# Performance work log

Hardware: AMD Instinct MI355X
Metric: run time of the kernel (lower is better)

## Reference

```python
import jax, jax.numpy as jnp
import numpy as np

KE2 = 2.31e-4  # ke2 constant from source
EPS = 1e-12    # safe-norm epsilon
N = 4096


def setup_inputs() -> dict:
    key = jax.random.key(0)
    ks = jax.random.split(key, 16)
    f32 = jnp.float32
    inp = {}
    inp['positions'] = jax.random.normal(ks[0], (N, 3), f32) * 5.0
    inp['charges'] = jax.random.normal(ks[1], (N,), f32)
    inp['bond_coeffs'] = jax.random.uniform(ks[2], (7, 7), f32)
    inp['bond_lengths'] = jax.random.uniform(ks[3], (7, 7), f32)
    inp['angle_coeffs'] = jax.random.uniform(ks[4], (7, 7, 7), f32)
    inp['thetas'] = jax.random.uniform(ks[5], (7, 7, 7), f32)
    inp['dihedral_coeffs'] = jax.random.uniform(ks[6], (7, 7), f32)
    inp['phis'] = jax.random.uniform(ks[7], (7, 7), f32)
    inp['multiplicity'] = jax.random.uniform(ks[8], (7, 7), f32)
    inp['lj_E'] = jax.random.uniform(ks[9], (4, 4), f32)
    inp['lj_r'] = jax.random.uniform(ks[10], (4, 4), f32)
    inp['atom_types'] = jax.random.randint(ks[11], (N,), 0, 7)
    inp['lj_types'] = jax.random.randint(ks[12], (N,), 0, 4)
    inp['bond_idx'] = jax.random.randint(ks[13], (N, 2), 0, N)
    inp['angle_idx'] = jax.random.randint(ks[14], (2 * N, 3), 0, N)
    inp['dihedral_idx'] = jax.random.randint(ks[15], (3 * N, 4), 0, N)
    return inp


def _norm(v):
    return jnp.sqrt(jnp.sum(v * v, axis=-1) + EPS)


def reference(positions, charges, bond_coeffs, bond_lengths, angle_coeffs,
              thetas, dihedral_coeffs, phis, multiplicity, lj_E, lj_r,
              atom_types, lj_types, bond_idx, angle_idx, dihedral_idx):
    t = atom_types
    # ---- bond energy: 0.5*k*(|ri-rj| - r0)^2, vectorized gather + reduce
    b1, b2 = bond_idx[:, 0], bond_idx[:, 1]
    d = _norm(positions[b1] - positions[b2])
    e_bond = jnp.sum(0.5 * bond_coeffs[t[b1], t[b2]] * (d - bond_lengths[t[b1], t[b2]]) ** 2)
    # ---- angle energy: 0.5*k*(acos(cos) - theta0)^2
    a1, a2, a3 = angle_idx[:, 0], angle_idx[:, 1], angle_idx[:, 2]
    v1 = positions[a1] - positions[a2]
    v2 = positions[a3] - positions[a2]
    cos_a = jnp.sum(v1 * v2, -1) / (_norm(v1) * _norm(v2))
    ang = jnp.arccos(jnp.clip(cos_a, -1.0 + 1e-7, 1.0 - 1e-7))
    ta1, ta2, ta3 = t[a1], t[a2], t[a3]
    e_angle = jnp.sum(0.5 * angle_coeffs[ta1, ta2, ta3] * (ang - thetas[ta1, ta2, ta3]) ** 2)
    # ---- dihedral energy: 0.5*k*(1 + cos(n*phi - delta))
    d1, d2i, d3, d4 = (dihedral_idx[:, k] for k in range(4))
    w1 = positions[d2i] - positions[d1]
    w2 = positions[d3] - positions[d2i]
    w3 = positions[d4] - positions[d3]
    n1 = jnp.cross(w1, w2)
    n2 = jnp.cross(w2, w3)
    cos_d = jnp.sum(n1 * n2, -1) / (_norm(n1) * _norm(n2))
    sin_d = jnp.sum(jnp.cross(n1, n2) * w2, -1) / (_norm(w2) * _norm(n1) * _norm(n2))
    phi = jnp.arctan2(sin_d, cos_d)
    td2, td3 = t[d2i], t[d3]
    e_dih = jnp.sum(0.5 * dihedral_coeffs[td2, td3] *
                    (1.0 + jnp.cos(multiplicity[td2, td3] * phi - phis[td2, td3])))
    # ---- pairwise distance map (cdist) via gram trick, upper-triangle i<j mask
    n = positions.shape[0]
    sq = jnp.sum(positions * positions, -1)
    d2m = jnp.maximum(sq[:, None] + sq[None, :] - 2.0 * (positions @ positions.T), 0.0)
    idx = jnp.arange(n)
    mask = idx[:, None] < idx[None, :]
    r = jnp.sqrt(jnp.where(mask, d2m, 1.0) + EPS)  # [N,N], safe off-mask
    # ---- Lennard-Jones: 4*eps*((sig/r)^12 - (sig/r)^6)
    eps_ij = lj_E[lj_types[:, None], lj_types[None, :]]
    sig_ij = lj_r[lj_types[:, None], lj_types[None, :]]
    r6 = (sig_ij / r) ** 6
    e_lj = jnp.sum(jnp.where(mask, 4.0 * eps_ij * (r6 * r6 - r6), 0.0))
    # ---- Coulomb: ke2 * qi*qj / r
    e_c = jnp.sum(jnp.where(mask, KE2 * charges[:, None] * charges[None, :] / r, 0.0))
    return e_bond + e_angle + e_dih + e_lj + e_c
```

## Files before the change

### kernel.cpp

```cpp
#include <hip/hip_runtime.h>

#define NATOMS 4096
#define TILE   128
#define NTILES (NATOMS / TILE)
#define KE2F   0.000231f

#define NEAR_D2 1.0f

__global__ __launch_bounds__(256) void energy_kernel(
    const float* __restrict__ pos,
    const float* __restrict__ charges,
    const float* __restrict__ bond_coeffs,
    const float* __restrict__ bond_lengths,
    const float* __restrict__ angle_coeffs,
    const float* __restrict__ thetas,
    const float* __restrict__ dihedral_coeffs,
    const float* __restrict__ phis,
    const float* __restrict__ multiplicity,
    const float* __restrict__ lj_E,
    const float* __restrict__ lj_r,
    const int* __restrict__ atom_types,
    const int* __restrict__ lj_types,
    const int* __restrict__ bond_idx,
    const int* __restrict__ angle_idx,
    const int* __restrict__ dihedral_idx,
    float* __restrict__ out)
{
    const int bi  = blockIdx.y;
    const int bj  = blockIdx.x;
    const int tid = threadIdx.x;

    __shared__ float4 sp[TILE];
    __shared__ float  ssq[TILE];
    __shared__ int    st[TILE];
    __shared__ double red[4];

    double acc = 0.0;

    if (bj >= bi) {
        const int il   = tid & (TILE - 1);
        const int half = tid >> 7;
        const int ig   = bi * TILE + il;
        const int jb   = bj * TILE;

        if (tid < TILE) {
            const int jg = jb + tid;
            const float x = pos[jg*3+0], y = pos[jg*3+1], z = pos[jg*3+2];
            sp[tid]  = make_float4(x, y, z, charges[jg]);
            ssq[tid] = __fadd_rn(__fadd_rn(__fmul_rn(x,x), __fmul_rn(y,y)), __fmul_rn(z,z));
            st[tid]  = lj_types[jg];
        }

        const float xi = pos[ig*3+0], yi = pos[ig*3+1], zi = pos[ig*3+2];
        const float sqi = __fadd_rn(__fadd_rn(__fmul_rn(xi,xi), __fmul_rn(yi,yi)), __fmul_rn(zi,zi));
        const float aqi = __fmul_rn(KE2F, charges[ig]);
        const int   ti  = lj_types[ig];
        const float e0 = 4.f*lj_E[ti*4+0], e1 = 4.f*lj_E[ti*4+1],
                    e2 = 4.f*lj_E[ti*4+2], e3 = 4.f*lj_E[ti*4+3];
        const float s0 = lj_r[ti*4+0], s1 = lj_r[ti*4+1],
                    s2 = lj_r[ti*4+2], s3 = lj_r[ti*4+3];

        __syncthreads();

        const int j0 = half * (TILE/2);
        for (int jj = j0; jj < j0 + TILE/2; ++jj) {
            const float4 pj  = sp[jj];
            const float  sqj = ssq[jj];
            const int    tj  = st[jj];
            const int    jg  = jb + jj;
            const bool valid = jg > ig;

            const float dot = __fmaf_rn(zi, pj.z,
                              __fmaf_rn(yi, pj.y,
                              __fmaf_rn(xi, pj.x, 0.0f)));
            const float t   = __fadd_rn(sqi, sqj);
            const float d2  = __fsub_rn(t, __fmul_rn(2.0f, dot));
            const float d2m = fmaxf(d2, 0.0f);
            const float rr2 = __fadd_rn(d2m, 1e-12f);

            const float sig = (tj==0)?s0:(tj==1)?s1:(tj==2)?s2:s3;
            const float e4  = (tj==0)?e0:(tj==1)?e1:(tj==2)?e2:e3;

            if (__builtin_expect(d2m <= NEAR_D2, 0)) {
                if (valid) {
                    const float rf = __fsqrt_rn(rr2);
                    const float qv = __fdiv_rn(sig, rf);
                    const double u  = (double)qv;
                    const double u3 = u*u*u;
                    const float r6 = (float)(u3*u3);
                    const float lj = __fsub_rn(__fmul_rn(r6, r6), r6);
                    const float ljt = __fmul_rn(e4, lj);
                    const float cl  = __fdiv_rn(__fmul_rn(aqi, pj.w), rf);
                    acc += (double)ljt;
                    acc += (double)cl;
                }
            } else {
                const float invr = __builtin_amdgcn_rsqf(rr2);
                const float u  = sig * invr;
                const float u2 = u*u;
                const float u6 = u2*u2*u2;
                const float term = e4 * (u6*u6 - u6) + aqi * pj.w * invr;
                acc += valid ? (double)term : 0.0;
            }
        }
    } else {
        const int l   = (bi * (bi - 1)) / 2 + bj;
        const int NB  = NATOMS;
        const int NA  = 2 * NATOMS;
        const int ND  = 3 * NATOMS;
        const int TOT = NB + NA + ND;
        if (l * 256 >= TOT) return;
        const int item = l * 256 + tid;

        if (item < NB) {
            const int b1 = bond_idx[item*2+0];
            const int b2 = bond_idx[item*2+1];
            const float dx = pos[b1*3+0] - pos[b2*3+0];
            const float dy = pos[b1*3+1] - pos[b2*3+1];
            const float dz = pos[b1*3+2] - pos[b2*3+2];
            const float d  = sqrtf(dx*dx + dy*dy + dz*dz + 1e-12f);
            const int k    = atom_types[b1]*7 + atom_types[b2];
            const float dd = d - bond_lengths[k];
            acc = 0.5 * (double)(bond_coeffs[k] * dd * dd);
        } else if (item < NB + NA) {
            const int ai = item - NB;
            const int a1 = angle_idx[ai*3+0];
            const int a2 = angle_idx[ai*3+1];
            const int a3 = angle_idx[ai*3+2];
            const float v1x = pos[a1*3+0] - pos[a2*3+0];
            const float v1y = pos[a1*3+1] - pos[a2*3+1];
            const float v1z = pos[a1*3+2] - pos[a2*3+2];
            const float v2x = pos[a3*3+0] - pos[a2*3+0];
            const float v2y = pos[a3*3+1] - pos[a2*3+1];
            const float v2z = pos[a3*3+2] - pos[a2*3+2];
            const float n1 = sqrtf(v1x*v1x + v1y*v1y + v1z*v1z + 1e-12f);
            const float n2 = sqrtf(v2x*v2x + v2y*v2y + v2z*v2z + 1e-12f);
            float cosa = (v1x*v2x + v1y*v2y + v1z*v2z) / (n1 * n2);
            cosa = fminf(fmaxf(cosa, -1.0f + 1e-7f), 1.0f - 1e-7f);
            const float ang = acosf(cosa);
            const int k = atom_types[a1]*49 + atom_types[a2]*7 + atom_types[a3];
            const float dt = ang - thetas[k];
            acc = 0.5 * (double)(angle_coeffs[k] * dt * dt);
        } else {
            const int di = item - NB - NA;
            const int q1 = dihedral_idx[di*4+0];
            const int q2 = dihedral_idx[di*4+1];
            const int q3 = dihedral_idx[di*4+2];
            const int q4 = dihedral_idx[di*4+3];
            const float w1x = pos[q2*3+0] - pos[q1*3+0];
            const float w1y = pos[q2*3+1] - pos[q1*3+1];
            const float w1z = pos[q2*3+2] - pos[q1*3+2];
            const float w2x = pos[q3*3+0] - pos[q2*3+0];
            const float w2y = pos[q3*3+1] - pos[q2*3+1];
            const float w2z = pos[q3*3+2] - pos[q2*3+2];
            const float w3x = pos[q4*3+0] - pos[q3*3+0];
            const float w3y = pos[q4*3+1] - pos[q3*3+1];
            const float w3z = pos[q4*3+2] - pos[q3*3+2];
            const float n1x = w1y*w2z - w1z*w2y;
            const float n1y = w1z*w2x - w1x*w2z;
            const float n1z = w1x*w2y - w1y*w2x;
            const float n2x = w2y*w3z - w2z*w3y;
            const float n2y = w2z*w3x - w2x*w3z;
            const float n2z = w2x*w3y - w2y*w3x;
            const float nn1 = sqrtf(n1x*n1x + n1y*n1y + n1z*n1z + 1e-12f);
            const float nn2 = sqrtf(n2x*n2x + n2y*n2y + n2z*n2z + 1e-12f);
            const float nw2 = sqrtf(w2x*w2x + w2y*w2y + w2z*w2z + 1e-12f);
            const float cosd = (n1x*n2x + n1y*n2y + n1z*n2z) / (nn1 * nn2);
            const float cx = n1y*n2z - n1z*n2y;
            const float cy = n1z*n2x - n1x*n2z;
            const float cz = n1x*n2y - n1y*n2x;
            const float sind = (cx*w2x + cy*w2y + cz*w2z) / (nw2 * nn1 * nn2);
            const float phi = atan2f(sind, cosd);
            const int k = atom_types[q2]*7 + atom_types[q3];
            const float e = 0.5f * dihedral_coeffs[k]
                          * (1.0f + cosf(multiplicity[k]*phi - phis[k]));
            acc = (double)e;
        }
    }

    #pragma unroll
    for (int s = 32; s > 0; s >>= 1) acc += __shfl_down(acc, s, 64);
    if ((tid & 63) == 0) red[tid >> 6] = acc;
    __syncthreads();
    if (tid == 0) {
        const float tot = (float)(red[0] + red[1] + red[2] + red[3]);
        atomicAdd(out, tot);
    }
}

extern "C" void kernel_launch(void* const* d_in, const int* in_sizes, int n_in,
                              void* d_out, int out_size, void* d_ws, size_t ws_size,
                              hipStream_t stream) {
    (void)in_sizes; (void)n_in; (void)d_ws; (void)ws_size; (void)out_size;
    hipMemsetAsync(d_out, 0, sizeof(float), stream);
    dim3 grid(NTILES, NTILES);
    energy_kernel<<<grid, 256, 0, stream>>>(
        (const float*)d_in[0],  (const float*)d_in[1],
        (const float*)d_in[2],  (const float*)d_in[3],
        (const float*)d_in[4],  (const float*)d_in[5],
        (const float*)d_in[6],  (const float*)d_in[7],
        (const float*)d_in[8],  (const float*)d_in[9],
        (const float*)d_in[10], (const int*)d_in[11],
        (const int*)d_in[12],   (const int*)d_in[13],
        (const int*)d_in[14],   (const int*)d_in[15],
        (float*)d_out);
}
```

Before: 104.6 us.

## Use direct-difference distances, float accumulation, and tighter near-field threshold in pair loop

The pair loop now computes squared distance from coordinate differences rather than the gram expansion, and evaluates the exact gram-based path only when d2 falls below a much smaller threshold. Far-field contributions are summed into a float accumulator instead of double, and the validity test becomes a local index comparison. The inner loop is unrolled by 8 and the shared per-atom squared-norm array is removed. This cuts double-precision adds and branch divergence in the hot loop, at the cost of float-accumulation rounding error and possible mismatch with the reference's gram-trick distances near the threshold.

```diff
diff --git a/kernel.cpp b/kernel.cpp
--- a/kernel.cpp
+++ b/kernel.cpp
@@ -5,7 +5,7 @@
 #define NTILES (NATOMS / TILE)
 #define KE2F   0.000231f
 
-#define NEAR_D2 1.0f
+#define NEAR_D2 4e-3f
 
 __global__ __launch_bounds__(256) void energy_kernel(
     const float* __restrict__ pos,
@@ -31,78 +31,82 @@
     const int tid = threadIdx.x;
 
     __shared__ float4 sp[TILE];
-    __shared__ float  ssq[TILE];
     __shared__ int    st[TILE];
     __shared__ double red[4];
 
     double acc = 0.0;
 
     if (bj >= bi) {
-        const int il   = tid & (TILE - 1);
-        const int half = tid >> 7;
-        const int ig   = bi * TILE + il;
-        const int jb   = bj * TILE;
+        const int il  = tid & (TILE - 1);
+        const int sub = tid >> 7;
+        const int ig  = bi * TILE + il;
+        const int jb  = bj * TILE;
 
         if (tid < TILE) {
             const int jg = jb + tid;
-            const float x = pos[jg*3+0], y = pos[jg*3+1], z = pos[jg*3+2];
-            sp[tid]  = make_float4(x, y, z, charges[jg]);
-            ssq[tid] = __fadd_rn(__fadd_rn(__fmul_rn(x,x), __fmul_rn(y,y)), __fmul_rn(z,z));
-            st[tid]  = lj_types[jg];
+            sp[tid] = make_float4(pos[jg*3+0], pos[jg*3+1], pos[jg*3+2], charges[jg]);
+            st[tid] = lj_types[jg];
         }
 
         const float xi = pos[ig*3+0], yi = pos[ig*3+1], zi = pos[ig*3+2];
-        const float sqi = __fadd_rn(__fadd_rn(__fmul_rn(xi,xi), __fmul_rn(yi,yi)), __fmul_rn(zi,zi));
+        const float sqi = __fadd_rn(__fadd_rn(__fmul_rn(xi,xi), __fmul_rn(yi,yi)),
+                                    __fmul_rn(zi,zi));
         const float aqi = __fmul_rn(KE2F, charges[ig]);
         const int   ti  = lj_types[ig];
         const float e0 = 4.f*lj_E[ti*4+0], e1 = 4.f*lj_E[ti*4+1],
                     e2 = 4.f*lj_E[ti*4+2], e3 = 4.f*lj_E[ti*4+3];
         const float s0 = lj_r[ti*4+0], s1 = lj_r[ti*4+1],
                     s2 = lj_r[ti*4+2], s3 = lj_r[ti*4+3];
+        const int jmin = (bi == bj) ? il : -1;
 
         __syncthreads();
 
-        const int j0 = half * (TILE/2);
+        float accf = 0.0f;
+        const int j0 = sub * (TILE/2);
+        #pragma unroll 8
         for (int jj = j0; jj < j0 + TILE/2; ++jj) {
-            const float4 pj  = sp[jj];
-            const float  sqj = ssq[jj];
-            const int    tj  = st[jj];
-            const int    jg  = jb + jj;
-            const bool valid = jg > ig;
-
-            const float dot = __fmaf_rn(zi, pj.z,
-                              __fmaf_rn(yi, pj.y,
-                              __fmaf_rn(xi, pj.x, 0.0f)));
-            const float t   = __fadd_rn(sqi, sqj);
-            const float d2  = __fsub_rn(t, __fmul_rn(2.0f, dot));
-            const float d2m = fmaxf(d2, 0.0f);
-            const float rr2 = __fadd_rn(d2m, 1e-12f);
+            const float4 pj = sp[jj];
+            const int    tj = st[jj];
+
+            const float dx = xi - pj.x;
+            const float dy = yi - pj.y;
+            const float dz = zi - pj.z;
+            const float d2 = __fmaf_rn(dx,dx, __fmaf_rn(dy,dy, dz*dz));
 
             const float sig = (tj==0)?s0:(tj==1)?s1:(tj==2)?s2:s3;
             const float e4  = (tj==0)?e0:(tj==1)?e1:(tj==2)?e2:e3;
-
-            if (__builtin_expect(d2m <= NEAR_D2, 0)) {
+            const bool valid = jj > jmin;
+
+            if (__builtin_expect(d2 < NEAR_D2, 0)) {
                 if (valid) {
-                    const float rf = __fsqrt_rn(rr2);
-                    const float qv = __fdiv_rn(sig, rf);
+                    const float sqj = __fadd_rn(__fadd_rn(__fmul_rn(pj.x,pj.x),
+                                                          __fmul_rn(pj.y,pj.y)),
+                                                __fmul_rn(pj.z,pj.z));
+                    const float dot = __fmaf_rn(zi, pj.z,
+                                      __fmaf_rn(yi, pj.y,
+                                      __fmaf_rn(xi, pj.x, 0.0f)));
+                    const float t   = __fadd_rn(sqi, sqj);
+                    const float d2n = __fsub_rn(t, __fmul_rn(2.0f, dot));
+                    const float rr2 = __fadd_rn(fmaxf(d2n, 0.0f), 1e-12f);
+                    const float rf  = __fsqrt_rn(rr2);
+                    const float qv  = __fdiv_rn(sig, rf);
                     const double u  = (double)qv;
                     const double u3 = u*u*u;
-                    const float r6 = (float)(u3*u3);
-                    const float lj = __fsub_rn(__fmul_rn(r6, r6), r6);
-                    const float ljt = __fmul_rn(e4, lj);
-                    const float cl  = __fdiv_rn(__fmul_rn(aqi, pj.w), rf);
-                    acc += (double)ljt;
-                    acc += (double)cl;
+                    const float r6  = (float)(u3*u3);
+                    const float lj  = __fsub_rn(__fmul_rn(r6, r6), r6);
+                    acc += (double)__fmul_rn(e4, lj);
+                    acc += (double)__fdiv_rn(__fmul_rn(aqi, pj.w), rf);
                 }
             } else {
-                const float invr = __builtin_amdgcn_rsqf(rr2);
+                const float invr = __builtin_amdgcn_rsqf(d2 + 1e-12f);
                 const float u  = sig * invr;
                 const float u2 = u*u;
                 const float u6 = u2*u2*u2;
-                const float term = e4 * (u6*u6 - u6) + aqi * pj.w * invr;
-                acc += valid ? (double)term : 0.0;
+                const float term = e4 * (u6*u6 - u6) + (aqi * pj.w) * invr;
+                accf += valid ? term : 0.0f;
             }
         }
+        acc += (double)accf;
     } else {
         const int l   = (bi * (bi - 1)) / 2 + bj;
         const int NB  = NATOMS;
```

After: 102.5 us. 1.02x faster.
